# Kernel optimization log

Measured on AMD Instinct MI355X. Metric: run time of the kernel, lower is better.

## Reference

```python
import jax, jax.numpy as jnp
import numpy as np

N = 8192
IN_DIM = 256
OUT_DIM = 256


def setup_inputs() -> dict:
    key = jax.random.key(0)
    k1, k2, k3, k4 = jax.random.split(key, 4)
    x = jax.random.normal(k1, (N, IN_DIM), dtype=jnp.float32)
    adj = jax.random.uniform(k2, (N, N), dtype=jnp.float32)
    # nn.Linear(in_dim, out_dim): weight [out,in], bias [out]. Store W as [in,out].
    bound = 1.0 / np.sqrt(IN_DIM)
    W = jax.random.uniform(k3, (IN_DIM, OUT_DIM), dtype=jnp.float32, minval=-bound, maxval=bound)
    b = jax.random.uniform(k4, (OUT_DIM,), dtype=jnp.float32, minval=-bound, maxval=bound)
    return {"x": x, "adj": adj, "W": W, "b": b}


def reference(x, adj, W, b):
    # ReLU( D^{-1/2} (A + I) D^{-1/2} X W + b )
    # A_hat = adj + I; degree = A_hat.sum(axis=1)
    n = adj.shape[0]
    A_hat = adj + jnp.eye(n, dtype=adj.dtype)
    degree = A_hat.sum(axis=1)
    d_inv_sqrt = degree ** -0.5  # [N]
    # D^{-1/2} @ A_hat @ D^{-1/2} == row-scale then col-scale (no NxN diag matmuls)
    A_norm = A_hat * d_inv_sqrt[:, None] * d_inv_sqrt[None, :]
    out = A_norm @ x          # [N, in_dim]
    out = out @ W + b         # [N, out_dim]
    return jax.nn.relu(out)
```

## Files before the change

kernel.cpp:

```cpp
#include <hip/hip_runtime.h>
#include <hip/hip_bf16.h>


typedef __attribute__((ext_vector_type(8))) short short8;
typedef __attribute__((ext_vector_type(4))) float floatx4;

#define GLDS16(g, l) __builtin_amdgcn_global_load_lds(\
    (const __attribute__((address_space(1))) void*)(g), \
    (__attribute__((address_space(3))) void*)(l), 16, 0, 0)

__device__ __forceinline__ unsigned short f2b(float f) {
  unsigned int x = __builtin_bit_cast(unsigned int, f);
  unsigned int r = (x + 0x7fffu + ((x >> 16) & 1u)) >> 16;
  return (unsigned short)r;
}

__global__ __launch_bounds__(256) void k_deg(
    const float* __restrict__ adj, float* __restrict__ degree) {
  const int t = threadIdx.x;
  const int row = blockIdx.x * 8 + (t >> 5);
  const int c = t & 31;
  const float* src = adj + (size_t)row * 8192 + c * 4;
  float rs = 0.f;
#pragma unroll 8
  for (int it = 0; it < 64; ++it) {
    float4 v = *(const float4*)(src + it * 128);
    rs += v.x + v.y + v.z + v.w;
  }
#pragma unroll
  for (int o = 16; o > 0; o >>= 1) rs += __shfl_down(rs, o, 32);
  if (c == 0) degree[row] = rs;
}

__global__ __launch_bounds__(256) void k_xw(
    const float* __restrict__ X, const float* __restrict__ W,
    const float* __restrict__ bias, const float* __restrict__ degree,
    float* __restrict__ Zd, unsigned short* __restrict__ Zsb) {
  __shared__ unsigned short ldsT[256 * 36];
  const int t = threadIdx.x, l = t & 63, w = t >> 6;
  const int m0 = blockIdx.x * 32;
  const int r0 = w * 8;
  const int n0 = l * 4;
  const float* Xp = X + (size_t)(m0 + r0) * 256;
  float acc[8][4] = {};
#pragma unroll 2
  for (int k = 0; k < 256; k += 4) {
    float4 wv[4];
#pragma unroll
    for (int j = 0; j < 4; ++j) wv[j] = *(const float4*)(W + (size_t)(k + j) * 256 + n0);
#pragma unroll
    for (int r = 0; r < 8; ++r) {
      float4 xv = *(const float4*)(Xp + r * 256 + k);
      const float xs[4] = {xv.x, xv.y, xv.z, xv.w};
#pragma unroll
      for (int j = 0; j < 4; ++j) {
        acc[r][0] += xs[j] * wv[j].x;
        acc[r][1] += xs[j] * wv[j].y;
        acc[r][2] += xs[j] * wv[j].z;
        acc[r][3] += xs[j] * wv[j].w;
      }
    }
  }
  const float4 bv = *(const float4*)(bias + n0);
  const int kt = m0 >> 6, hh = (m0 >> 5) & 1;
#pragma unroll
  for (int r = 0; r < 8; ++r) {
    const int row = m0 + r0 + r;
    const float sr = rsqrtf(degree[row] + 1.0f);
    float4 zd;
    zd.x = sr * sr * acc[r][0] + bv.x;
    zd.y = sr * sr * acc[r][1] + bv.y;
    zd.z = sr * sr * acc[r][2] + bv.z;
    zd.w = sr * sr * acc[r][3] + bv.w;
    *(float4*)(Zd + (size_t)row * 256 + n0) = zd;
#pragma unroll
    for (int n = 0; n < 4; ++n)
      ldsT[(size_t)(n0 + n) * 36 + (r0 + r)] = f2b(sr * acc[r][n]);
  }
  __syncthreads();
#pragma unroll
  for (int c = 0; c < 4; ++c) {
    const int kcv = hh * 4 + c;
    const unsigned short* p = ldsT + (size_t)t * 36 + c * 8;
    short8 vv;
#pragma unroll
    for (int j = 0; j < 8; ++j) vv[j] = p[j];
    *(short8*)(Zsb + ((size_t)kt * 2048 + kcv * 256 + t) * 8) = vv;
  }
}

__global__ __launch_bounds__(512) void k_main(
    const float* __restrict__ adj, const unsigned short* __restrict__ Zsb,
    float* __restrict__ P) {
  __shared__ __align__(16) char lds[2][20608];
  const int t = threadIdx.x, l = t & 63, w = t >> 6;
  const int quad = l >> 4, nl = l & 15;
  const int bm = blockIdx.x >> 2, sk = blockIdx.x & 3;
  const int m0 = bm * 64;
  const int wm = w & 1, wn = w >> 1;
  const int aRow = t >> 3, aCol = t & 7;
  const float* aSrc = adj + (size_t)(m0 + aRow) * 8192 + sk * 2048 + aCol * 4;
  const int aOff = (aCol >> 1) * 1040 + aRow * 16 + (aCol & 1) * 8;
  const unsigned short* bBase = Zsb + (size_t)sk * 65536 * 8;
  floatx4 acc[2][4] = {};

  float4 avP = *(const float4*)(aSrc);
#pragma unroll
  for (int q = 0; q < 2; ++q) {
    const int sl = q * 512 + t;
    GLDS16(bBase + (size_t)sl * 8, lds[0] + 4224 + sl * 16);
  }
  {
    unsigned short u0 = f2b(avP.x), u1 = f2b(avP.y), u2 = f2b(avP.z), u3 = f2b(avP.w);
    unsigned long long pk = (unsigned long long)u0 | ((unsigned long long)u1 << 16)
                          | ((unsigned long long)u2 << 32) | ((unsigned long long)u3 << 48);
    *(unsigned long long*)(lds[0] + aOff) = pk;
  }
  avP = *(const float4*)(aSrc + 32);
  __syncthreads();

  for (int i = 0; i < 64; ++i) {
    const int cur = i & 1, nxt = cur ^ 1;
    const int ib = i < 63 ? i + 1 : 63;
    const int ia = i < 62 ? i + 2 : 63;
#pragma unroll
    for (int q = 0; q < 2; ++q) {
      const int sl = q * 512 + t;
      GLDS16(bBase + (size_t)(ib * 1024 + sl) * 8, lds[nxt] + 4224 + sl * 16);
    }
    float4 avN = *(const float4*)(aSrc + ia * 32);
    const char* rA = lds[cur];
    const char* rB = lds[cur] + 4224;
    short8 af[2], bf[4];
    af[0] = *(const short8*)(rA + quad * 1040 + (wm * 32 + nl) * 16);
    af[1] = *(const short8*)(rA + quad * 1040 + (wm * 32 + 16 + nl) * 16);
#pragma unroll
    for (int nf = 0; nf < 4; ++nf) {
      const int col = wn * 64 + nf * 16 + nl;
      bf[nf] = *(const short8*)(rB + ((size_t)quad * 256 + col) * 16);
    }
#pragma unroll
    for (int mi = 0; mi < 2; ++mi)
#pragma unroll
      for (int nf = 0; nf < 4; ++nf)
        acc[mi][nf] = __builtin_amdgcn_mfma_f32_16x16x32_bf16(af[mi], bf[nf], acc[mi][nf], 0, 0, 0);
    {
      unsigned short u0 = f2b(avP.x), u1 = f2b(avP.y), u2 = f2b(avP.z), u3 = f2b(avP.w);
      unsigned long long pk = (unsigned long long)u0 | ((unsigned long long)u1 << 16)
                            | ((unsigned long long)u2 << 32) | ((unsigned long long)u3 << 48);
      *(unsigned long long*)(lds[nxt] + aOff) = pk;
    }
    avP = avN;
    __syncthreads();
  }

  float* Pk = P + (size_t)sk * 8192 * 256;
#pragma unroll
  for (int mi = 0; mi < 2; ++mi)
#pragma unroll
    for (int nf = 0; nf < 4; ++nf)
#pragma unroll
      for (int r = 0; r < 4; ++r) {
        const int row = m0 + wm * 32 + mi * 16 + quad * 4 + r;
        const int col = wn * 64 + nf * 16 + nl;
        Pk[(size_t)row * 256 + col] = acc[mi][nf][r];
      }
}

__global__ __launch_bounds__(256) void k_fin(
    const float* __restrict__ P, const float* __restrict__ Zd,
    const float* __restrict__ degree, float* __restrict__ out) {
  const int i = blockIdx.x * 256 + threadIdx.x;
  const int row = i >> 6;
  const float sr = rsqrtf(degree[row] + 1.0f);
  const size_t stride = (size_t)8192 * 256;
  float4 p0 = *(const float4*)(P + (size_t)i * 4);
  float4 p1 = *(const float4*)(P + stride + (size_t)i * 4);
  float4 p2 = *(const float4*)(P + 2 * stride + (size_t)i * 4);
  float4 p3 = *(const float4*)(P + 3 * stride + (size_t)i * 4);
  const float4 zd = *(const float4*)(Zd + (size_t)i * 4);
  float4 v;
  v.x = sr * ((p0.x + p1.x) + (p2.x + p3.x)) + zd.x;
  v.y = sr * ((p0.y + p1.y) + (p2.y + p3.y)) + zd.y;
  v.z = sr * ((p0.z + p1.z) + (p2.z + p3.z)) + zd.z;
  v.w = sr * ((p0.w + p1.w) + (p2.w + p3.w)) + zd.w;
  v.x = v.x > 0.f ? v.x : 0.f;
  v.y = v.y > 0.f ? v.y : 0.f;
  v.z = v.z > 0.f ? v.z : 0.f;
  v.w = v.w > 0.f ? v.w : 0.f;
  *(float4*)(out + (size_t)i * 4) = v;
}

extern "C" void kernel_launch(void* const* d_in, const int* in_sizes, int n_in,
                              void* d_out, int out_size, void* d_ws, size_t ws_size,
                              hipStream_t stream) {
  const float* X    = (const float*)d_in[0];
  const float* adj  = (const float*)d_in[1];
  const float* W    = (const float*)d_in[2];
  const float* bias = (const float*)d_in[3];
  float* out = (float*)d_out;
  char* ws = (char*)d_ws;

  float* degree       = (float*)(ws);
  float* Zd           = (float*)(ws + (1 << 20));
  unsigned short* Zsb = (unsigned short*)(ws + (9 << 20));
  float* P            = (float*)(ws + (13 << 20));

  hipLaunchKernelGGL(k_deg, dim3(1024), dim3(256), 0, stream, adj, degree);
  hipLaunchKernelGGL(k_xw, dim3(256), dim3(256), 0, stream, X, W, bias, degree, Zd, Zsb);
  hipLaunchKernelGGL(k_main, dim3(512), dim3(512), 0, stream, adj, Zsb, P);
  hipLaunchKernelGGL(k_fin, dim3(2048), dim3(256), 0, stream, P, Zd, degree, out);
}
```

Measured before the change: 508.4 us.

## Convert adjacency to pre-tiled bf16 in degree pass, feed main GEMM via direct LDS loads

The degree kernel now also converts adj to bf16 and writes it in the MFMA tile layout, producing per-split partial degrees. The main GEMM then loads A with global_load_lds asynchronously instead of loading fp32 through registers and converting inside the loop. This takes conversion work and register staging out of the GEMM's critical path. The cost is an extra 128 MB bf16 write and read of adj in exchange for halving the fp32 A read in the main kernel. k_xw is re-tiled to 16 rows per block and also stores the inverse square-root degree for k_fin.

```diff
diff --git a/kernel.cpp b/kernel.cpp
--- a/kernel.cpp
+++ b/kernel.cpp
@@ -1,5 +1,4 @@
 #include <hip/hip_runtime.h>
-#include <hip/hip_bf16.h>
 
 
 typedef __attribute__((ext_vector_type(8))) short short8;
@@ -15,41 +14,58 @@
   return (unsigned short)r;
 }
 
-__global__ __launch_bounds__(256) void k_deg(
-    const float* __restrict__ adj, float* __restrict__ degree) {
-  const int t = threadIdx.x;
-  const int row = blockIdx.x * 8 + (t >> 5);
-  const int c = t & 31;
-  const float* src = adj + (size_t)row * 8192 + c * 4;
+__global__ __launch_bounds__(512) void k_deg(
+    const float* __restrict__ adj, unsigned short* __restrict__ adjb,
+    float* __restrict__ degree4) {
+  __shared__ float part[8][64];
+  const int t = threadIdx.x, l = t & 63, w = t >> 6;
+  const int mb = blockIdx.x >> 2, sk = blockIdx.x & 3;
+  const int m0 = mb * 64;
+  const float* src = adj + (size_t)(m0 + l) * 8192 + sk * 2048;
+  unsigned short* dstBase = adjb + ((size_t)(mb * 4 + sk) * 16384 + l) * 8;
   float rs = 0.f;
-#pragma unroll 8
-  for (int it = 0; it < 64; ++it) {
-    float4 v = *(const float4*)(src + it * 128);
-    rs += v.x + v.y + v.z + v.w;
-  }
-#pragma unroll
-  for (int o = 16; o > 0; o >>= 1) rs += __shfl_down(rs, o, 32);
-  if (c == 0) degree[row] = rs;
+  for (int i = w * 8; i < w * 8 + 8; ++i) {
+    const float* s = src + i * 32;
+#pragma unroll
+    for (int q = 0; q < 4; ++q) {
+      float4 v0 = *(const float4*)(s + q * 8);
+      float4 v1 = *(const float4*)(s + q * 8 + 4);
+      short8 u;
+      u[0] = f2b(v0.x); u[1] = f2b(v0.y); u[2] = f2b(v0.z); u[3] = f2b(v0.w);
+      u[4] = f2b(v1.x); u[5] = f2b(v1.y); u[6] = f2b(v1.z); u[7] = f2b(v1.w);
+      *(short8*)(dstBase + (size_t)(i * 4 + q) * 512) = u;
+      rs += ((v0.x + v0.y) + (v0.z + v0.w)) + ((v1.x + v1.y) + (v1.z + v1.w));
+    }
+  }
+  part[w][l] = rs;
+  __syncthreads();
+  if (t < 64) {
+    float s = 0.f;
+#pragma unroll
+    for (int ww = 0; ww < 8; ++ww) s += part[ww][t];
+    degree4[sk * 8192 + m0 + t] = s;
+  }
 }
 
 __global__ __launch_bounds__(256) void k_xw(
     const float* __restrict__ X, const float* __restrict__ W,
-    const float* __restrict__ bias, const float* __restrict__ degree,
-    float* __restrict__ Zd, unsigned short* __restrict__ Zsb) {
-  __shared__ unsigned short ldsT[256 * 36];
+    const float* __restrict__ bias, const float* __restrict__ degree4,
+    float* __restrict__ Zd, unsigned short* __restrict__ Zsb,
+    float* __restrict__ sinv) {
+  __shared__ unsigned short ldsT[256 * 20];
   const int t = threadIdx.x, l = t & 63, w = t >> 6;
-  const int m0 = blockIdx.x * 32;
-  const int r0 = w * 8;
+  const int m0 = blockIdx.x * 16;
+  const int r0 = w * 4;
   const int n0 = l * 4;
   const float* Xp = X + (size_t)(m0 + r0) * 256;
-  float acc[8][4] = {};
+  float acc[4][4] = {};
 #pragma unroll 2
   for (int k = 0; k < 256; k += 4) {
     float4 wv[4];
 #pragma unroll
     for (int j = 0; j < 4; ++j) wv[j] = *(const float4*)(W + (size_t)(k + j) * 256 + n0);
 #pragma unroll
-    for (int r = 0; r < 8; ++r) {
+    for (int r = 0; r < 4; ++r) {
       float4 xv = *(const float4*)(Xp + r * 256 + k);
       const float xs[4] = {xv.x, xv.y, xv.z, xv.w};
 #pragma unroll
@@ -62,11 +78,13 @@
     }
   }
   const float4 bv = *(const float4*)(bias + n0);
-  const int kt = m0 >> 6, hh = (m0 >> 5) & 1;
-#pragma unroll
-  for (int r = 0; r < 8; ++r) {
+#pragma unroll
+  for (int r = 0; r < 4; ++r) {
     const int row = m0 + r0 + r;
-    const float sr = rsqrtf(degree[row] + 1.0f);
+    const float deg = degree4[row] + degree4[8192 + row]
+                    + degree4[16384 + row] + degree4[24576 + row];
+    const float sr = rsqrtf(deg + 1.0f);
+    if (l == 0) sinv[row] = sr;
     float4 zd;
     zd.x = sr * sr * acc[r][0] + bv.x;
     zd.y = sr * sr * acc[r][1] + bv.y;
@@ -75,22 +93,22 @@
     *(float4*)(Zd + (size_t)row * 256 + n0) = zd;
 #pragma unroll
     for (int n = 0; n < 4; ++n)
-      ldsT[(size_t)(n0 + n) * 36 + (r0 + r)] = f2b(sr * acc[r][n]);
+      ldsT[(size_t)(n0 + n) * 20 + (r0 + r)] = f2b(sr * acc[r][n]);
   }
   __syncthreads();
-#pragma unroll
-  for (int c = 0; c < 4; ++c) {
-    const int kcv = hh * 4 + c;
-    const unsigned short* p = ldsT + (size_t)t * 36 + c * 8;
+  const int kt = m0 >> 6, kcb = (m0 >> 3) & 7;
+#pragma unroll
+  for (int c = 0; c < 2; ++c) {
+    const unsigned short* p = ldsT + (size_t)t * 20 + c * 8;
     short8 vv;
 #pragma unroll
     for (int j = 0; j < 8; ++j) vv[j] = p[j];
-    *(short8*)(Zsb + ((size_t)kt * 2048 + kcv * 256 + t) * 8) = vv;
+    *(short8*)(Zsb + ((size_t)kt * 2048 + (kcb + c) * 256 + t) * 8) = vv;
   }
 }
 
 __global__ __launch_bounds__(512) void k_main(
-    const float* __restrict__ adj, const unsigned short* __restrict__ Zsb,
+    const unsigned short* __restrict__ adjb, const unsigned short* __restrict__ Zsb,
     float* __restrict__ P) {
   __shared__ __align__(16) char lds[2][20608];
   const int t = threadIdx.x, l = t & 63, w = t >> 6;
@@ -98,37 +116,30 @@
   const int bm = blockIdx.x >> 2, sk = blockIdx.x & 3;
   const int m0 = bm * 64;
   const int wm = w & 1, wn = w >> 1;
-  const int aRow = t >> 3, aCol = t & 7;
-  const float* aSrc = adj + (size_t)(m0 + aRow) * 8192 + sk * 2048 + aCol * 4;
-  const int aOff = (aCol >> 1) * 1040 + aRow * 16 + (aCol & 1) * 8;
-  const unsigned short* bBase = Zsb + (size_t)sk * 65536 * 8;
+  const unsigned short* aBase = adjb + (size_t)(bm * 4 + sk) * 131072;
+  const unsigned short* bBase = Zsb + (size_t)sk * 524288;
   floatx4 acc[2][4] = {};
 
-  float4 avP = *(const float4*)(aSrc);
+  if (t < 256)
+    GLDS16(aBase + (size_t)t * 8, lds[0] + (t >> 6) * 1040 + (t & 63) * 16);
 #pragma unroll
   for (int q = 0; q < 2; ++q) {
     const int sl = q * 512 + t;
     GLDS16(bBase + (size_t)sl * 8, lds[0] + 4224 + sl * 16);
   }
-  {
-    unsigned short u0 = f2b(avP.x), u1 = f2b(avP.y), u2 = f2b(avP.z), u3 = f2b(avP.w);
-    unsigned long long pk = (unsigned long long)u0 | ((unsigned long long)u1 << 16)
-                          | ((unsigned long long)u2 << 32) | ((unsigned long long)u3 << 48);
-    *(unsigned long long*)(lds[0] + aOff) = pk;
-  }
-  avP = *(const float4*)(aSrc + 32);
   __syncthreads();
 
   for (int i = 0; i < 64; ++i) {
     const int cur = i & 1, nxt = cur ^ 1;
     const int ib = i < 63 ? i + 1 : 63;
-    const int ia = i < 62 ? i + 2 : 63;
+    if (t < 256)
+      GLDS16(aBase + ((size_t)ib * 256 + t) * 8,
+             lds[nxt] + (t >> 6) * 1040 + (t & 63) * 16);
 #pragma unroll
     for (int q = 0; q < 2; ++q) {
       const int sl = q * 512 + t;
-      GLDS16(bBase + (size_t)(ib * 1024 + sl) * 8, lds[nxt] + 4224 + sl * 16);
-    }
-    float4 avN = *(const float4*)(aSrc + ia * 32);
+      GLDS16(bBase + ((size_t)ib * 1024 + sl) * 8, lds[nxt] + 4224 + sl * 16);
+    }
     const char* rA = lds[cur];
     const char* rB = lds[cur] + 4224;
     short8 af[2], bf[4];
@@ -144,13 +155,6 @@
 #pragma unroll
       for (int nf = 0; nf < 4; ++nf)
         acc[mi][nf] = __builtin_amdgcn_mfma_f32_16x16x32_bf16(af[mi], bf[nf], acc[mi][nf], 0, 0, 0);
-    {
-      unsigned short u0 = f2b(avP.x), u1 = f2b(avP.y), u2 = f2b(avP.z), u3 = f2b(avP.w);
-      unsigned long long pk = (unsigned long long)u0 | ((unsigned long long)u1 << 16)
-                            | ((unsigned long long)u2 << 32) | ((unsigned long long)u3 << 48);
-      *(unsigned long long*)(lds[nxt] + aOff) = pk;
-    }
-    avP = avN;
     __syncthreads();
   }
 
@@ -169,10 +173,10 @@
 
 __global__ __launch_bounds__(256) void k_fin(
     const float* __restrict__ P, const float* __restrict__ Zd,
-    const float* __restrict__ degree, float* __restrict__ out) {
+    const float* __restrict__ sinv, float* __restrict__ out) {
   const int i = blockIdx.x * 256 + threadIdx.x;
   const int row = i >> 6;
-  const float sr = rsqrtf(degree[row] + 1.0f);
+  const float sr = sinv[row];
   const size_t stride = (size_t)8192 * 256;
   float4 p0 = *(const float4*)(P + (size_t)i * 4);
   float4 p1 = *(const float4*)(P + stride + (size_t)i * 4);
@@ -201,13 +205,15 @@
   float* out = (float*)d_out;
   char* ws = (char*)d_ws;
 
-  float* degree       = (float*)(ws);
-  float* Zd           = (float*)(ws + (1 << 20));
-  unsigned short* Zsb = (unsigned short*)(ws + (9 << 20));
-  float* P            = (float*)(ws + (13 << 20));
-
-  hipLaunchKernelGGL(k_deg, dim3(1024), dim3(256), 0, stream, adj, degree);
-  hipLaunchKernelGGL(k_xw, dim3(256), dim3(256), 0, stream, X, W, bias, degree, Zd, Zsb);
-  hipLaunchKernelGGL(k_main, dim3(512), dim3(512), 0, stream, adj, Zsb, P);
-  hipLaunchKernelGGL(k_fin, dim3(2048), dim3(256), 0, stream, P, Zd, degree, out);
-}
+  float* degree4       = (float*)(ws);
+  float* sinv          = (float*)(ws + (256 << 10));
+  float* Zd            = (float*)(ws + (1 << 20));
+  unsigned short* Zsb  = (unsigned short*)(ws + (9 << 20));
+  float* P             = (float*)(ws + (13 << 20));
+  unsigned short* adjb = (unsigned short*)(ws + (45 << 20));
+
+  hipLaunchKernelGGL(k_deg,  dim3(512),  dim3(512), 0, stream, adj, adjb, degree4);
+  hipLaunchKernelGGL(k_xw,   dim3(512),  dim3(256), 0, stream, X, W, bias, degree4, Zd, Zsb, sinv);
+  hipLaunchKernelGGL(k_main, dim3(512),  dim3(512), 0, stream, adjb, Zsb, P);
+  hipLaunchKernelGGL(k_fin,  dim3(2048), dim3(256), 0, stream, P, Zd, sinv, out);
+}
```

Result: slower. 529.4 us (+4.1%).

## Restructure main loop sync with manual waitcnts and split XW across more blocks

Applied to the files above, without the earlier changes.

Replaces the end-of-iteration __syncthreads in the main adj×Z loop with a top-of-loop barrier guarded by explicit vmcnt/lgkmcnt waits. The next A tile's LDS write now comes before the MFMAs, which run at raised priority, so global loads can stay in flight across iterations. The XW kernel is halved per block (16 rows, 512 blocks) to raise parallelism, and the degree kernel now stores rsqrt directly. Hand-tuned waitcnt counts risk races if the compiler reorders or issues a different number of memory ops.

```diff
diff --git a/kernel.cpp b/kernel.cpp
--- a/kernel.cpp
+++ b/kernel.cpp
@@ -1,5 +1,4 @@
 #include <hip/hip_runtime.h>
-#include <hip/hip_bf16.h>
 
 
 typedef __attribute__((ext_vector_type(8))) short short8;
@@ -8,6 +7,11 @@
 #define GLDS16(g, l) __builtin_amdgcn_global_load_lds(\
     (const __attribute__((address_space(1))) void*)(g), \
     (__attribute__((address_space(3))) void*)(l), 16, 0, 0)
+
+#define VMW1  asm volatile("s_waitcnt vmcnt(1)" ::: "memory")
+#define VMW3  asm volatile("s_waitcnt vmcnt(3)" ::: "memory")
+#define VMW0  asm volatile("s_waitcnt vmcnt(0)" ::: "memory")
+#define LGKM0 asm volatile("s_waitcnt lgkmcnt(0)" ::: "memory")
 
 __device__ __forceinline__ unsigned short f2b(float f) {
   unsigned int x = __builtin_bit_cast(unsigned int, f);
@@ -16,7 +20,7 @@
 }
 
 __global__ __launch_bounds__(256) void k_deg(
-    const float* __restrict__ adj, float* __restrict__ degree) {
+    const float* __restrict__ adj, float* __restrict__ sinv) {
   const int t = threadIdx.x;
   const int row = blockIdx.x * 8 + (t >> 5);
   const int c = t & 31;
@@ -29,27 +33,27 @@
   }
 #pragma unroll
   for (int o = 16; o > 0; o >>= 1) rs += __shfl_down(rs, o, 32);
-  if (c == 0) degree[row] = rs;
+  if (c == 0) sinv[row] = rsqrtf(rs + 1.0f);
 }
 
 __global__ __launch_bounds__(256) void k_xw(
     const float* __restrict__ X, const float* __restrict__ W,
-    const float* __restrict__ bias, const float* __restrict__ degree,
+    const float* __restrict__ bias, const float* __restrict__ sinv,
     float* __restrict__ Zd, unsigned short* __restrict__ Zsb) {
-  __shared__ unsigned short ldsT[256 * 36];
+  __shared__ unsigned short ldsT[256 * 20];
   const int t = threadIdx.x, l = t & 63, w = t >> 6;
-  const int m0 = blockIdx.x * 32;
-  const int r0 = w * 8;
+  const int m0 = blockIdx.x * 16;
+  const int r0 = w * 4;
   const int n0 = l * 4;
   const float* Xp = X + (size_t)(m0 + r0) * 256;
-  float acc[8][4] = {};
+  float acc[4][4] = {};
 #pragma unroll 2
   for (int k = 0; k < 256; k += 4) {
     float4 wv[4];
 #pragma unroll
     for (int j = 0; j < 4; ++j) wv[j] = *(const float4*)(W + (size_t)(k + j) * 256 + n0);
 #pragma unroll
-    for (int r = 0; r < 8; ++r) {
+    for (int r = 0; r < 4; ++r) {
       float4 xv = *(const float4*)(Xp + r * 256 + k);
       const float xs[4] = {xv.x, xv.y, xv.z, xv.w};
 #pragma unroll
@@ -62,11 +66,10 @@
     }
   }
   const float4 bv = *(const float4*)(bias + n0);
-  const int kt = m0 >> 6, hh = (m0 >> 5) & 1;
-#pragma unroll
-  for (int r = 0; r < 8; ++r) {
+#pragma unroll
+  for (int r = 0; r < 4; ++r) {
     const int row = m0 + r0 + r;
-    const float sr = rsqrtf(degree[row] + 1.0f);
+    const float sr = sinv[row];
     float4 zd;
     zd.x = sr * sr * acc[r][0] + bv.x;
     zd.y = sr * sr * acc[r][1] + bv.y;
@@ -75,17 +78,17 @@
     *(float4*)(Zd + (size_t)row * 256 + n0) = zd;
 #pragma unroll
     for (int n = 0; n < 4; ++n)
-      ldsT[(size_t)(n0 + n) * 36 + (r0 + r)] = f2b(sr * acc[r][n]);
+      ldsT[(size_t)(n0 + n) * 20 + (r0 + r)] = f2b(sr * acc[r][n]);
   }
   __syncthreads();
-#pragma unroll
-  for (int c = 0; c < 4; ++c) {
-    const int kcv = hh * 4 + c;
-    const unsigned short* p = ldsT + (size_t)t * 36 + c * 8;
+  const int kt = m0 >> 6, kcb = (m0 >> 3) & 7;
+#pragma unroll
+  for (int c = 0; c < 2; ++c) {
+    const unsigned short* p = ldsT + (size_t)t * 20 + c * 8;
     short8 vv;
 #pragma unroll
     for (int j = 0; j < 8; ++j) vv[j] = p[j];
-    *(short8*)(Zsb + ((size_t)kt * 2048 + kcv * 256 + t) * 8) = vv;
+    *(short8*)(Zsb + ((size_t)kt * 2048 + (kcb + c) * 256 + t) * 8) = vv;
   }
 }
 
@@ -104,31 +107,45 @@
   const unsigned short* bBase = Zsb + (size_t)sk * 65536 * 8;
   floatx4 acc[2][4] = {};
 
-  float4 avP = *(const float4*)(aSrc);
 #pragma unroll
   for (int q = 0; q < 2; ++q) {
     const int sl = q * 512 + t;
     GLDS16(bBase + (size_t)sl * 8, lds[0] + 4224 + sl * 16);
   }
+  float4 avP = *(const float4*)(aSrc);
+  float4 avN = *(const float4*)(aSrc + 32);
   {
     unsigned short u0 = f2b(avP.x), u1 = f2b(avP.y), u2 = f2b(avP.z), u3 = f2b(avP.w);
     unsigned long long pk = (unsigned long long)u0 | ((unsigned long long)u1 << 16)
                           | ((unsigned long long)u2 << 32) | ((unsigned long long)u3 << 48);
     *(unsigned long long*)(lds[0] + aOff) = pk;
   }
-  avP = *(const float4*)(aSrc + 32);
-  __syncthreads();
-
+  avP = avN;
+
+#pragma unroll 2
   for (int i = 0; i < 64; ++i) {
     const int cur = i & 1, nxt = cur ^ 1;
     const int ib = i < 63 ? i + 1 : 63;
     const int ia = i < 62 ? i + 2 : 63;
+    VMW1;
+    LGKM0;
+    __builtin_amdgcn_s_barrier();
+    __builtin_amdgcn_sched_barrier(0);
 #pragma unroll
     for (int q = 0; q < 2; ++q) {
       const int sl = q * 512 + t;
       GLDS16(bBase + (size_t)(ib * 1024 + sl) * 8, lds[nxt] + 4224 + sl * 16);
     }
-    float4 avN = *(const float4*)(aSrc + ia * 32);
+    avN = *(const float4*)(aSrc + ia * 32);
+    VMW3;
+    __builtin_amdgcn_sched_barrier(0);
+    {
+      unsigned short u0 = f2b(avP.x), u1 = f2b(avP.y), u2 = f2b(avP.z), u3 = f2b(avP.w);
+      unsigned long long pk = (unsigned long long)u0 | ((unsigned long long)u1 << 16)
+                            | ((unsigned long long)u2 << 32) | ((unsigned long long)u3 << 48);
+      *(unsigned long long*)(lds[nxt] + aOff) = pk;
+    }
+    avP = avN;
     const char* rA = lds[cur];
     const char* rB = lds[cur] + 4224;
     short8 af[2], bf[4];
@@ -139,20 +156,15 @@
       const int col = wn * 64 + nf * 16 + nl;
       bf[nf] = *(const short8*)(rB + ((size_t)quad * 256 + col) * 16);
     }
+    __builtin_amdgcn_s_setprio(1);
 #pragma unroll
     for (int mi = 0; mi < 2; ++mi)
 #pragma unroll
       for (int nf = 0; nf < 4; ++nf)
         acc[mi][nf] = __builtin_amdgcn_mfma_f32_16x16x32_bf16(af[mi], bf[nf], acc[mi][nf], 0, 0, 0);
-    {
-      unsigned short u0 = f2b(avP.x), u1 = f2b(avP.y), u2 = f2b(avP.z), u3 = f2b(avP.w);
-      unsigned long long pk = (unsigned long long)u0 | ((unsigned long long)u1 << 16)
-                            | ((unsigned long long)u2 << 32) | ((unsigned long long)u3 << 48);
-      *(unsigned long long*)(lds[nxt] + aOff) = pk;
-    }
-    avP = avN;
-    __syncthreads();
-  }
+    __builtin_amdgcn_s_setprio(0);
+  }
+  VMW0;
 
   float* Pk = P + (size_t)sk * 8192 * 256;
 #pragma unroll
@@ -169,10 +181,10 @@
 
 __global__ __launch_bounds__(256) void k_fin(
     const float* __restrict__ P, const float* __restrict__ Zd,
-    const float* __restrict__ degree, float* __restrict__ out) {
+    const float* __restrict__ sinv, float* __restrict__ out) {
   const int i = blockIdx.x * 256 + threadIdx.x;
   const int row = i >> 6;
-  const float sr = rsqrtf(degree[row] + 1.0f);
+  const float sr = sinv[row];
   const size_t stride = (size_t)8192 * 256;
   float4 p0 = *(const float4*)(P + (size_t)i * 4);
   float4 p1 = *(const float4*)(P + stride + (size_t)i * 4);
@@ -201,13 +213,13 @@
   float* out = (float*)d_out;
   char* ws = (char*)d_ws;
 
-  float* degree       = (float*)(ws);
-  float* Zd           = (float*)(ws + (1 << 20));
-  unsigned short* Zsb = (unsigned short*)(ws + (9 << 20));
-  float* P            = (float*)(ws + (13 << 20));
-
-  hipLaunchKernelGGL(k_deg, dim3(1024), dim3(256), 0, stream, adj, degree);
-  hipLaunchKernelGGL(k_xw, dim3(256), dim3(256), 0, stream, X, W, bias, degree, Zd, Zsb);
-  hipLaunchKernelGGL(k_main, dim3(512), dim3(512), 0, stream, adj, Zsb, P);
-  hipLaunchKernelGGL(k_fin, dim3(2048), dim3(256), 0, stream, P, Zd, degree, out);
-}
+  float* sinv          = (float*)(ws);
+  float* Zd            = (float*)(ws + (1 << 20));
+  unsigned short* Zsb  = (unsigned short*)(ws + (9 << 20));
+  float* P             = (float*)(ws + (13 << 20));
+
+  hipLaunchKernelGGL(k_deg,  dim3(1024), dim3(256), 0, stream, adj, sinv);
+  hipLaunchKernelGGL(k_xw,   dim3(512),  dim3(256), 0, stream, X, W, bias, sinv, Zd, Zsb);
+  hipLaunchKernelGGL(k_main, dim3(512),  dim3(512), 0, stream, adj, Zsb, P);
+  hipLaunchKernelGGL(k_fin,  dim3(2048), dim3(256), 0, stream, P, Zd, sinv, out);
+}
```

Measured after the change: 517.6 us. About the same (+1.8%).
